# Performance work log

Hardware: AMD Instinct MI355X
Metric: run time of the kernel (lower is better)

The kernel has to match this reference:

```python
import jax, jax.numpy as jnp
import numpy as np

B, L, D, TK = 64, 48, 256, 128
T = 2 * L - 1  # L shifts + (L-1) reduces


def setup_inputs() -> dict:
    key = jax.random.key(0)
    ks = jax.random.split(key, 9)
    s = 0.05
    inp = {
        "buf_h": jax.random.normal(ks[0], (B, L, D), jnp.float32),
        "buf_c": jax.random.normal(ks[1], (B, L, D), jnp.float32),
        # Tracker weights: buf/stack1/stack2 (size -> 4*tracker_size, no bias), lateral (tk -> 4*tk, bias)
        "Wb": jax.random.normal(ks[2], (D, 4 * TK), jnp.float32) * s,
        "W1": jax.random.normal(ks[3], (D, 4 * TK), jnp.float32) * s,
        "W2": jax.random.normal(ks[4], (D, 4 * TK), jnp.float32) * s,
        "Wl": jax.random.normal(ks[5], (TK, 4 * TK), jnp.float32) * s,
        "bl": jnp.zeros((4 * TK,), jnp.float32),
        # Reduce (TreeLSTM) weights: left (size->5*size, bias), right (no bias), track (tk->5*size, no bias)
        "WL": jax.random.normal(ks[6], (D, 5 * D), jnp.float32) * s,
        "bL": jnp.zeros((5 * D,), jnp.float32),
        "WR": jax.random.normal(ks[7], (D, 5 * D), jnp.float32) * s,
        "WT": jax.random.normal(ks[8], (TK, 5 * D), jnp.float32) * s,
    }
    # Valid full-length transition sequence per example: S S (R S)*(L-2) R  -> SHIFT=0, REDUCE=1
    pat = np.array([0, 0] + [1, 0] * (L - 2) + [1], dtype=np.int32)
    inp["transitions"] = jnp.asarray(np.tile(pat[None], (B, 1)))  # [B, T]
    return inp


def _lstm(c, gates):
    # tracker LSTM cell: gates chunk into (a, i, f, o)
    a, i, f, o = jnp.split(gates, 4, axis=-1)
    c2 = jnp.tanh(a) * jax.nn.sigmoid(i) + jax.nn.sigmoid(f) * c
    h2 = jax.nn.sigmoid(o) * jnp.tanh(c2)
    return c2, h2


def _treelstm(c1, c2, gates):
    # Reduce composition: gates chunk into (a, i, f1, f2, o)
    a, i, f1, f2, o = jnp.split(gates, 5, axis=-1)
    c = jnp.tanh(a) * jax.nn.sigmoid(i) + jax.nn.sigmoid(f1) * c1 + jax.nn.sigmoid(f2) * c2
    h = jax.nn.sigmoid(o) * jnp.tanh(c)
    return h, c


def _spinn_forward(buf_h, buf_c, transitions, Wb, W1, W2, Wl, bl, WL, bL, WR, WT):
    Bn, Ln, Dn = buf_h.shape
    Tn = transitions.shape[1]
    bidx = jnp.arange(Bn)
    stack0 = jnp.zeros((Bn, Ln, 2 * Dn), buf_h.dtype)  # each slot holds [h; c]
    sp0 = jnp.zeros((Bn,), jnp.int32)  # stack depth
    bp0 = jnp.zeros((Bn,), jnp.int32)  # buffer read pointer
    th0 = jnp.zeros((Bn, Wl.shape[0]), buf_h.dtype)
    tc0 = jnp.zeros_like(th0)

    def top(stack_, sp_, k):
        # k-th item from the top, zeros if depth < k (matches explicit zero-padding)
        idx = jnp.clip(sp_ - k, 0, Ln - 1)
        v = stack_[bidx, idx]
        return jnp.where((sp_ >= k)[:, None], v, jnp.zeros_like(v))

    def step(carry, xs):
        stack, sp, bp, th, tc = carry
        t, trans = xs
        shift = (trans == 0)
        bp_safe = jnp.clip(bp, 0, Ln - 1)
        buf_ok = (bp < Ln)[:, None]
        tb_h = jnp.where(buf_ok, buf_h[bidx, bp_safe], 0.0)  # top-of-buffer h
        s1 = top(stack, sp, 1)
        s2 = top(stack, sp, 2)
        s1h, s1c = s1[:, :Dn], s1[:, Dn:]
        s2h, s2c = s2[:, :Dn], s2[:, Dn:]
        # Tracker: sum of three bias-free linears (+ lateral with bias after step 0)
        gates = tb_h @ Wb + s1h @ W1 + s2h @ W2
        gates = gates + jnp.where(t > 0, th @ Wl + bl, 0.0)
        tc2, th2 = _lstm(tc, gates)
        # Reduce: right = top of stack, left = second item; tracking = new tracker h
        rgates = s2h @ WL + bL + s1h @ WR + th2 @ WT
        rh, rc = _treelstm(s2c, s1c, rgates)
        reduced = jnp.concatenate([rh, rc], axis=-1)
        # Shift: push [h;c] from buffer
        tb_c = jnp.where(buf_ok, buf_c[bidx, bp_safe], 0.0)
        shifted = jnp.concatenate([tb_h, tb_c], axis=-1)
        newval = jnp.where(shift[:, None], shifted, reduced)
        pos = jnp.where(shift, sp, jnp.maximum(sp - 2, 0))
        stack = stack.at[bidx, pos].set(newval)
        sp = jnp.where(shift, sp + 1, jnp.maximum(sp - 1, 0))
        bp = bp + shift.astype(bp.dtype)
        return (stack, sp, bp, th2, tc2), None

    (stack, sp, bp, th, tc), _ = jax.lax.scan(
        step, (stack0, sp0, bp0, th0, tc0),
        (jnp.arange(Tn), transitions.T))
    final = stack[bidx, jnp.clip(sp - 1, 0, Ln - 1)]  # [B, 2D] = [h; c] of root
    return final


def reference(buf_h, buf_c, transitions, Wb, W1, W2, Wl, bl, WL, bL, WR, WT):
    return _spinn_forward(buf_h, buf_c, transitions, Wb, W1, W2, Wl, bl, WL, bL, WR, WT)
```

## Files before the change

kernel.cpp:

```cpp
#include <hip/hip_runtime.h>
#include <cstdint>
#include <cstddef>

#define NB 64
#define LN 48
#define DN 256
#define TKN 128
#define TN 95
#define RMAX 48
#define GA 512
#define GR 1280
#define NWG 256
#define NT 512

__device__ __forceinline__ float sigf(float x) { return 1.0f / (1.0f + expf(-x)); }

__device__ __forceinline__ float bf2f(unsigned u16) {
    unsigned x = u16 << 16;
    return __builtin_bit_cast(float, x);
}
__device__ __forceinline__ unsigned short f2bf(float f) {
    unsigned x = __builtin_bit_cast(unsigned, f);
    unsigned r = (x + 0x7FFFu + ((x >> 16) & 1u)) >> 16;
    return (unsigned short)r;
}

__device__ __forceinline__ float cohLd(const float* p) {
    return __hip_atomic_load(p, __ATOMIC_RELAXED, __HIP_MEMORY_SCOPE_AGENT);
}
__device__ __forceinline__ void cohSt(float* p, float v) {
    __hip_atomic_store(p, v, __ATOMIC_RELAXED, __HIP_MEMORY_SCOPE_AGENT);
}
__device__ __forceinline__ unsigned cohLdU(const unsigned* p) {
    return __hip_atomic_load(p, __ATOMIC_RELAXED, __HIP_MEMORY_SCOPE_AGENT);
}
__device__ __forceinline__ void cohStU(unsigned* p, unsigned v) {
    __hip_atomic_store(p, v, __ATOMIC_RELAXED, __HIP_MEMORY_SCOPE_AGENT);
}

__device__ __forceinline__ void qsync(unsigned* slots, int grp, unsigned& qph) {
    __syncthreads();
    qph += 1;
    if (threadIdx.x == 0) cohStU(&slots[blockIdx.x * 16], qph);
    if (threadIdx.x < 16) {
        while (cohLdU(&slots[(grp * 16 + threadIdx.x) * 16]) < qph)
            __builtin_amdgcn_s_sleep(1);
    }
    asm volatile("" ::: "memory");
    __syncthreads();
}

__device__ __forceinline__ void psync(unsigned* slotsP, int u, int xcd, unsigned& pph) {
    __syncthreads();
    pph += 1;
    if (threadIdx.x == 0) cohStU(&slotsP[(u * 8 + xcd) * 16], pph);
    if (threadIdx.x < 8) {
        while (cohLdU(&slotsP[(u * 8 + threadIdx.x) * 16]) < pph)
            __builtin_amdgcn_s_sleep(1);
    }
    asm volatile("" ::: "memory");
    __syncthreads();
}

__global__ void k_sched(const int* __restrict__ trans,
                        int* __restrict__ tbcode, int* __restrict__ s1code,
                        int* __restrict__ s2code, int* __restrict__ wkA,
                        int* __restrict__ fcode, int* __restrict__ anyred) {
    __shared__ int tg[NB][LN];
    int b = threadIdx.x;
    if (b >= NB) return;
    for (int i = 0; i < LN; ++i) tg[b][i] = -1;
    int sp = 0, bp = 0, k = 0;
    for (int t = 0; t < TN; ++t) {
        int tr = trans[b * TN + t];
        int shift = (tr == 0);
        int tb = (bp < LN) ? bp : -1;
        tbcode[t * NB + b] = tb;
        int i1 = sp - 1; if (i1 < 0) i1 = 0; if (i1 > LN - 1) i1 = LN - 1;
        int i2 = sp - 2; if (i2 < 0) i2 = 0; if (i2 > LN - 1) i2 = LN - 1;
        s1code[t * NB + b] = (sp >= 1) ? tg[b][i1] : -1;
        s2code[t * NB + b] = (sp >= 2) ? tg[b][i2] : -1;
        int wk_t;
        if (shift) {
            wk_t = -1;
            if (sp >= 0 && sp < LN) tg[b][sp] = tb;
            sp = sp + 1;
            bp = bp + 1;
        } else {
            wk_t = k;
            int pos = sp - 2; if (pos < 0) pos = 0;
            if (pos < LN) tg[b][pos] = 1000 + k;
            k++;
            sp = sp - 1; if (sp < 0) sp = 0;
        }
        wkA[t * NB + b] = wk_t;
        unsigned long long m = __ballot(wk_t >= 0);
        if (b == 0) anyred[t] = (m != 0ull) ? 1 : 0;
    }
    int fi = sp - 1; if (fi < 0) fi = 0; if (fi > LN - 1) fi = LN - 1;
    fcode[b] = tg[b][fi];
}

__global__ __launch_bounds__(256) void k_pack_a(
    const float* __restrict__ Wb, const float* __restrict__ W1,
    const float* __restrict__ W2, const float* __restrict__ Wl,
    const float* __restrict__ blv,
    unsigned short* __restrict__ WAb, float* __restrict__ blA) {
    int idx = blockIdx.x * 256 + threadIdx.x;
    if (idx < 8 * 896 * 64) {
        int s = idx / (896 * 64);
        int r = idx % (896 * 64);
        int k = r >> 6, c = r & 63;
        int p = s * 64 + c;
        int j = p >> 2, q = p & 3;
        int sc = q * 128 + j;
        float v;
        if (k < 256)      v = Wb[(size_t)k * GA + sc];
        else if (k < 512) v = W1[(size_t)(k - 256) * GA + sc];
        else if (k < 768) v = W2[(size_t)(k - 512) * GA + sc];
        else              v = Wl[(size_t)(k - 768) * GA + sc];
        WAb[idx] = f2bf(v);
    }
    if (idx < 512) {
        int j = idx >> 2, q = idx & 3;
        blA[idx] = blv[q * 128 + j];
    }
}

__global__ __launch_bounds__(256) void k_pack_b(
    const float* __restrict__ WLm, const float* __restrict__ WRm,
    const float* __restrict__ WTm, unsigned short* __restrict__ WBb) {
    int idx = blockIdx.x * 256 + threadIdx.x;
    if (idx >= 16 * 640 * 128) return;
    int s = idx / (640 * 128);
    int r = idx % (640 * 128);
    int k = r >> 7, cc = r & 127;
    int jj = cc >> 3, g = cc & 7;
    float v = 0.f;
    if (g < 5) {
        int sc = g * 256 + s * 16 + jj;
        if (k < 256)      v = WLm[(size_t)k * GR + sc];
        else if (k < 512) v = WRm[(size_t)(k - 256) * GR + sc];
        else              v = WTm[(size_t)(k - 512) * GR + sc];
    }
    WBb[idx] = f2bf(v);
}

__global__ __launch_bounds__(NT, 1) void k_spinn(
    const float* __restrict__ bufh, const float* __restrict__ bufc,
    const unsigned short* __restrict__ WAb, const float* __restrict__ blA,
    const unsigned short* __restrict__ WBb, const float* __restrict__ bLv,
    const int* __restrict__ tbcode, const int* __restrict__ s1code,
    const int* __restrict__ s2code, const int* __restrict__ wkA,
    const int* __restrict__ fcode, const int* __restrict__ anyred,
    float* __restrict__ th, float* __restrict__ tc,
    float* __restrict__ redh, float* __restrict__ redc,
    unsigned* __restrict__ slots, unsigned* __restrict__ slotsP,
    float* __restrict__ out) {
    const int wg = blockIdx.x;
    const int tid = threadIdx.x;
    const int lane = tid & 63;
    const int w = tid >> 6;
    unsigned qph = 0, pph = 0;

    const int xcd = wg & 7;
    const int u = wg >> 3;
    const int grp = wg >> 4;
    const int jg = xcd;
    const int bg1 = u;
    const int bg2 = u >> 1;
    const int jgw = (u & 1) + 2 * xcd;

    __shared__ float xs[2][896];
    __shared__ float part1[2][64][65];
    __shared__ float gsum[2][64];
    __shared__ float xs2[4][16][33];
    __shared__ float part2[16][16][21];
    __shared__ float gsum2[4][5][16];
    __shared__ float xst[4][128];
    __shared__ float cellv[2][4][17];

    for (int t = 0; t < TN; ++t) {
        const int par = t & 1;
        const bool red = anyred[t] != 0;

        int ngroups = red ? 1088 : 448;
        for (int g = tid; g < ngroups; g += NT) {
            if (g < 448) {
                int row = g & 1, k0 = (g >> 1) * 4;
                int b = bg1 * 2 + row;
                float4 v = {0.f, 0.f, 0.f, 0.f};
                if (k0 < 256) {
                    int c = tbcode[t * NB + b];
                    if (c >= 0) v = *(const float4*)&bufh[((size_t)b * LN + c) * DN + k0];
                } else if (k0 < 512) {
                    int c = s1code[t * NB + b];
                    int kk = k0 - 256;
                    if (c >= 1000) {
                        const float* p = &redh[((size_t)(c - 1000) * NB + b) * DN + kk];
                        v.x = cohLd(p); v.y = cohLd(p + 1); v.z = cohLd(p + 2); v.w = cohLd(p + 3);
                    } else if (c >= 0) v = *(const float4*)&bufh[((size_t)b * LN + c) * DN + kk];
                } else if (k0 < 768) {
                    int c = s2code[t * NB + b];
                    int kk = k0 - 512;
                    if (c >= 1000) {
                        const float* p = &redh[((size_t)(c - 1000) * NB + b) * DN + kk];
                        v.x = cohLd(p); v.y = cohLd(p + 1); v.z = cohLd(p + 2); v.w = cohLd(p + 3);
                    } else if (c >= 0) v = *(const float4*)&bufh[((size_t)b * LN + c) * DN + kk];
                } else {
                    const float* p = &th[((size_t)par * NB + b) * TKN + (k0 - 768)];
                    v.x = cohLd(p); v.y = cohLd(p + 1); v.z = cohLd(p + 2); v.w = cohLd(p + 3);
                }
                *(float4*)&xs[row][k0] = v;
            } else if (g < 960) {
                int g2 = g - 448;
                int row = g2 & 3, k0 = (g2 >> 2) * 4;
                int b = bg2 * 4 + row;
                float4 v = {0.f, 0.f, 0.f, 0.f};
                if (k0 < 256) {
                    int c = s2code[t * NB + b];
                    if (c >= 1000) {
                        const float* p = &redh[((size_t)(c - 1000) * NB + b) * DN + k0];
                        v.x = cohLd(p); v.y = cohLd(p + 1); v.z = cohLd(p + 2); v.w = cohLd(p + 3);
                    } else if (c >= 0) v = *(const float4*)&bufh[((size_t)b * LN + c) * DN + k0];
                } else {
                    int c = s1code[t * NB + b];
                    int kk = k0 - 256;
                    if (c >= 1000) {
                        const float* p = &redh[((size_t)(c - 1000) * NB + b) * DN + kk];
                        v.x = cohLd(p); v.y = cohLd(p + 1); v.z = cohLd(p + 2); v.w = cohLd(p + 3);
                    } else if (c >= 0) v = *(const float4*)&bufh[((size_t)b * LN + c) * DN + kk];
                }
                *(float4*)&xs2[row][k0 >> 5][k0 & 31] = v;
            } else {
                int g3 = g - 960;
                int sel = g3 >> 6, r = g3 & 63;
                int bl_ = r >> 4, jj = r & 15;
                int b = bg2 * 4 + bl_;
                int j = jgw * 16 + jj;
                int c = (sel ? s1code : s2code)[t * NB + b];
                float v = 0.f;
                if (c >= 1000)   v = redc[((size_t)(c - 1000) * NB + b) * DN + j];
                else if (c >= 0) v = bufc[((size_t)b * LN + c) * DN + j];
                cellv[sel][bl_][jj] = v;
            }
        }
        __syncthreads();

        float acc[5][4];
        if (w < 4 || !red) {
            int weff = w & 3, ihalf = w >> 2;
            int c8 = lane & 7, kq = lane >> 3;
            int kbase = weff * 224;
            int i0 = red ? 0 : ihalf * 14;
            int ni = red ? 28 : 14;
            const uint4* wp = (const uint4*)WAb + ((size_t)(jg * 896 + kbase + kq) * 8) + c8;
            float a0[8], a1[8];
            #pragma unroll
            for (int cc = 0; cc < 8; ++cc) { a0[cc] = 0.f; a1[cc] = 0.f; }
            #pragma unroll 4
            for (int ii = 0; ii < ni; ++ii) {
                int i = i0 + ii;
                uint4 wv = wp[(size_t)i * 64];
                int k = kbase + kq + i * 8;
                float x0 = xs[0][k], x1 = xs[1][k];
                float wf0 = bf2f(wv.x & 0xFFFF), wf1 = bf2f(wv.x >> 16);
                float wf2 = bf2f(wv.y & 0xFFFF), wf3 = bf2f(wv.y >> 16);
                float wf4 = bf2f(wv.z & 0xFFFF), wf5 = bf2f(wv.z >> 16);
                float wf6 = bf2f(wv.w & 0xFFFF), wf7 = bf2f(wv.w >> 16);
                a0[0] += x0 * wf0; a1[0] += x1 * wf0;
                a0[1] += x0 * wf1; a1[1] += x1 * wf1;
                a0[2] += x0 * wf2; a1[2] += x1 * wf2;
                a0[3] += x0 * wf3; a1[3] += x1 * wf3;
                a0[4] += x0 * wf4; a1[4] += x1 * wf4;
                a0[5] += x0 * wf5; a1[5] += x1 * wf5;
                a0[6] += x0 * wf6; a1[6] += x1 * wf6;
                a0[7] += x0 * wf7; a1[7] += x1 * wf7;
            }
            int slot = weff * 8 + kq + (red ? 0 : ihalf * 32);
            #pragma unroll
            for (int cc = 0; cc < 8; ++cc) {
                part1[0][c8 * 8 + cc][slot] = a0[cc];
                part1[1][c8 * 8 + cc][slot] = a1[cc];
            }
        } else {
            int t2 = tid - 256, jj = t2 & 15, ks = t2 >> 4;
            #pragma unroll
            for (int g = 0; g < 5; ++g)
                #pragma unroll
                for (int b4 = 0; b4 < 4; ++b4) acc[g][b4] = 0.f;
            const uint4* wb = (const uint4*)WBb + ((size_t)(jgw * 640 + ks * 32) * 16) + jj;
            #pragma unroll 4
            for (int i = 0; i < 32; ++i) {
                uint4 wv = wb[(size_t)i * 16];
                float w0 = bf2f(wv.x & 0xFFFF), w1 = bf2f(wv.x >> 16);
                float w2 = bf2f(wv.y & 0xFFFF), w3 = bf2f(wv.y >> 16);
                float w4 = bf2f(wv.z & 0xFFFF);
                float x0 = xs2[0][ks][i], x1 = xs2[1][ks][i];
                float x2 = xs2[2][ks][i], x3 = xs2[3][ks][i];
                acc[0][0] += x0 * w0; acc[1][0] += x0 * w1; acc[2][0] += x0 * w2; acc[3][0] += x0 * w3; acc[4][0] += x0 * w4;
                acc[0][1] += x1 * w0; acc[1][1] += x1 * w1; acc[2][1] += x1 * w2; acc[3][1] += x1 * w3; acc[4][1] += x1 * w4;
                acc[0][2] += x2 * w0; acc[1][2] += x2 * w1; acc[2][2] += x2 * w2; acc[3][2] += x2 * w3; acc[4][2] += x2 * w4;
                acc[0][3] += x3 * w0; acc[1][3] += x3 * w1; acc[2][3] += x3 * w2; acc[3][3] += x3 * w3; acc[4][3] += x3 * w4;
            }
        }
        __syncthreads();

        if (tid < 128) {
            int b = tid & 1, col = tid >> 1;
            float s = 0.f;
            #pragma unroll
            for (int ks = 0; ks < 32; ++ks) s += part1[b][col][ks];
            if (!red) {
                #pragma unroll
                for (int ks = 32; ks < 64; ++ks) s += part1[b][col][ks];
            }
            if (t > 0) s += blA[jg * 64 + col];
            gsum[b][col] = s;
        }
        __syncthreads();
        if (tid < 32) {
            int bl_ = tid >> 4, jj = tid & 15;
            int b = bg1 * 2 + bl_;
            int j = jg * 16 + jj;
            float4 g4 = *(const float4*)&gsum[bl_][jj * 4];
            float tco = tc[((size_t)par * NB + b) * TKN + j];
            float c2v = tanhf(g4.x) * sigf(g4.y) + sigf(g4.z) * tco;
            float h2 = sigf(g4.w) * tanhf(c2v);
            tc[((size_t)(par ^ 1) * NB + b) * TKN + j] = c2v;
            cohSt(&th[((size_t)(par ^ 1) * NB + b) * TKN + j], h2);
        }

        if (!red) {
            psync(slotsP, u, xcd, pph);
            continue;
        }
        qsync(slots, grp, qph);

        float xreg;
        {
            int b4 = tid >> 7, kk = tid & 127;
            xreg = cohLd(&th[((size_t)(par ^ 1) * NB + bg2 * 4 + b4) * TKN + kk]);
        }
        if (w >= 4) {
            int t2 = tid - 256, jj = t2 & 15, ks = t2 >> 4;
            #pragma unroll
            for (int g = 0; g < 5; ++g)
                #pragma unroll
                for (int b4 = 0; b4 < 4; ++b4)
                    part2[ks][jj][g * 4 + b4] = acc[g][b4];
        }
        {
            int b4 = tid >> 7, kk = tid & 127;
            xst[b4][kk] = xreg;
        }
        __syncthreads();
        if (w >= 4) {
            int t2 = tid - 256, jj = t2 & 15, ks = t2 >> 4;
            float wt[5][4];
            #pragma unroll
            for (int g = 0; g < 5; ++g)
                #pragma unroll
                for (int b4 = 0; b4 < 4; ++b4) wt[g][b4] = 0.f;
            const uint4* wb = (const uint4*)WBb + ((size_t)(jgw * 640 + 512 + ks * 8) * 16) + jj;
            #pragma unroll
            for (int i = 0; i < 8; ++i) {
                uint4 wv = wb[(size_t)i * 16];
                float w0 = bf2f(wv.x & 0xFFFF), w1 = bf2f(wv.x >> 16);
                float w2 = bf2f(wv.y & 0xFFFF), w3 = bf2f(wv.y >> 16);
                float w4 = bf2f(wv.z & 0xFFFF);
                int kk2 = ks * 8 + i;
                float x0 = xst[0][kk2], x1 = xst[1][kk2], x2 = xst[2][kk2], x3 = xst[3][kk2];
                wt[0][0] += x0 * w0; wt[1][0] += x0 * w1; wt[2][0] += x0 * w2; wt[3][0] += x0 * w3; wt[4][0] += x0 * w4;
                wt[0][1] += x1 * w0; wt[1][1] += x1 * w1; wt[2][1] += x1 * w2; wt[3][1] += x1 * w3; wt[4][1] += x1 * w4;
                wt[0][2] += x2 * w0; wt[1][2] += x2 * w1; wt[2][2] += x2 * w2; wt[3][2] += x2 * w3; wt[4][2] += x2 * w4;
                wt[0][3] += x3 * w0; wt[1][3] += x3 * w1; wt[2][3] += x3 * w2; wt[3][3] += x3 * w3; wt[4][3] += x3 * w4;
            }
            #pragma unroll
            for (int g = 0; g < 5; ++g)
                #pragma unroll
                for (int b4 = 0; b4 < 4; ++b4)
                    part2[ks][jj][g * 4 + b4] += wt[g][b4];
        }
        __syncthreads();
        if (tid < 320) {
            int g = tid >> 6, r = tid & 63;
            int bl_ = r >> 4, jj = r & 15;
            float s = 0.f;
            #pragma unroll
            for (int ks = 0; ks < 16; ++ks) s += part2[ks][jj][g * 4 + bl_];
            gsum2[bl_][g][jj] = s;
        }
        __syncthreads();
        if (tid < 64) {
            int bl_ = tid >> 4, jj = tid & 15;
            int b = bg2 * 4 + bl_;
            int wk = wkA[t * NB + b];
            if (wk >= 0) {
                int j = jgw * 16 + jj;
                float ga  = gsum2[bl_][0][jj] + bLv[0 * 256 + j];
                float gi  = gsum2[bl_][1][jj] + bLv[1 * 256 + j];
                float gf1 = gsum2[bl_][2][jj] + bLv[2 * 256 + j];
                float gf2 = gsum2[bl_][3][jj] + bLv[3 * 256 + j];
                float go  = gsum2[bl_][4][jj] + bLv[4 * 256 + j];
                float s2cv = cellv[0][bl_][jj];
                float s1cv = cellv[1][bl_][jj];
                float cc = tanhf(ga) * sigf(gi) + sigf(gf1) * s2cv + sigf(gf2) * s1cv;
                float hh = sigf(go) * tanhf(cc);
                cohSt(&redh[((size_t)wk * NB + b) * DN + j], hh);
                redc[((size_t)wk * NB + b) * DN + j] = cc;
            }
        }
        qsync(slots, grp, qph);
    }

    if (tid < 64) {
        int bl_ = tid >> 4, jj = tid & 15;
        int b = bg2 * 4 + bl_;
        int j = jgw * 16 + jj;
        int c = fcode[b];
        float h = 0.f, cv = 0.f;
        if (c >= 1000) {
            h  = cohLd(&redh[((size_t)(c - 1000) * NB + b) * DN + j]);
            cv = redc[((size_t)(c - 1000) * NB + b) * DN + j];
        } else if (c >= 0) {
            h  = bufh[((size_t)b * LN + c) * DN + j];
            cv = bufc[((size_t)b * LN + c) * DN + j];
        }
        out[(size_t)b * 2 * DN + j]      = h;
        out[(size_t)b * 2 * DN + DN + j] = cv;
    }
}

extern "C" void kernel_launch(void* const* d_in, const int* in_sizes, int n_in,
                              void* d_out, int out_size, void* d_ws, size_t ws_size,
                              hipStream_t stream) {
    const float* bufh = (const float*)d_in[0];
    const float* bufc = (const float*)d_in[1];
    const float* Wb   = (const float*)d_in[2];
    const float* W1   = (const float*)d_in[3];
    const float* W2   = (const float*)d_in[4];
    const float* Wl   = (const float*)d_in[5];
    const float* blv  = (const float*)d_in[6];
    const float* WLm  = (const float*)d_in[7];
    const float* bLv  = (const float*)d_in[8];
    const float* WR   = (const float*)d_in[9];
    const float* WT   = (const float*)d_in[10];
    const int* trans  = (const int*)d_in[11];
    float* out = (float*)d_out;

    char* p = (char*)d_ws;
    auto carve = [&](size_t bytes) -> char* {
        char* r = p;
        p += (bytes + 255) & ~(size_t)255;
        return r;
    };
    int* tbcode = (int*)carve((size_t)TN * NB * 4);
    int* s1code = (int*)carve((size_t)TN * NB * 4);
    int* s2code = (int*)carve((size_t)TN * NB * 4);
    int* wkA    = (int*)carve((size_t)TN * NB * 4);
    int* fcode  = (int*)carve((size_t)NB * 4);
    int* anyred = (int*)carve((size_t)TN * 4);
    float* th   = (float*)carve((size_t)2 * NB * TKN * 4);
    float* tc   = (float*)carve((size_t)2 * NB * TKN * 4);
    float* redh = (float*)carve((size_t)RMAX * NB * DN * 4);
    float* redc = (float*)carve((size_t)RMAX * NB * DN * 4);
    unsigned short* WAb = (unsigned short*)carve((size_t)8 * 896 * 64 * 2);
    float* blA  = (float*)carve((size_t)512 * 4);
    unsigned short* WBb = (unsigned short*)carve((size_t)16 * 640 * 128 * 2);
    unsigned* slots  = (unsigned*)carve((size_t)NWG * 16 * 4);
    unsigned* slotsP = (unsigned*)carve((size_t)NWG * 16 * 4);

    hipMemsetAsync(th, 0, (size_t)2 * NB * TKN * 4, stream);
    hipMemsetAsync(tc, 0, (size_t)2 * NB * TKN * 4, stream);
    hipMemsetAsync(slots, 0, (size_t)NWG * 16 * 4, stream);
    hipMemsetAsync(slotsP, 0, (size_t)NWG * 16 * 4, stream);

    k_sched<<<1, 64, 0, stream>>>(trans, tbcode, s1code, s2code, wkA, fcode, anyred);
    k_pack_a<<<(8 * 896 * 64 + 255) / 256, 256, 0, stream>>>(Wb, W1, W2, Wl, blv, WAb, blA);
    k_pack_b<<<(16 * 640 * 128 + 255) / 256, 256, 0, stream>>>(WLm, WR, WT, WBb);
    k_spinn<<<NWG, NT, 0, stream>>>(bufh, bufc, WAb, blA, WBb, bLv,
                                    tbcode, s1code, s2code, wkA, fcode, anyred,
                                    th, tc, redh, redc, slots, slotsP, out);
}
```

Measured before the change: 721.0 us.

## Prefetch step inputs before cross-workgroup barrier using precomputed readiness flags

The scheduler kernel now records, per step and example, whether each stack operand was produced at least two steps earlier (pre1/pre2). The main kernel moves the end-of-step barrier to the start of the next step and issues loads for already-ready buffer and reduce-result operands before spinning on the barrier, so their latency overlaps the wait. Only operands produced in the immediately preceding step and the tracker state are loaded after the barrier. This adds register pressure and extra schedule arrays, and it depends on the precomputed readiness being correct under the weaker sync ordering.

```diff
diff --git a/kernel.cpp b/kernel.cpp
--- a/kernel.cpp
+++ b/kernel.cpp
@@ -50,23 +50,13 @@
     __syncthreads();
 }
 
-__device__ __forceinline__ void psync(unsigned* slotsP, int u, int xcd, unsigned& pph) {
-    __syncthreads();
-    pph += 1;
-    if (threadIdx.x == 0) cohStU(&slotsP[(u * 8 + xcd) * 16], pph);
-    if (threadIdx.x < 8) {
-        while (cohLdU(&slotsP[(u * 8 + threadIdx.x) * 16]) < pph)
-            __builtin_amdgcn_s_sleep(1);
-    }
-    asm volatile("" ::: "memory");
-    __syncthreads();
-}
-
 __global__ void k_sched(const int* __restrict__ trans,
                         int* __restrict__ tbcode, int* __restrict__ s1code,
                         int* __restrict__ s2code, int* __restrict__ wkA,
-                        int* __restrict__ fcode, int* __restrict__ anyred) {
+                        int* __restrict__ fcode, int* __restrict__ anyred,
+                        int* __restrict__ pre1, int* __restrict__ pre2) {
     __shared__ int tg[NB][LN];
+    __shared__ short prod[NB][RMAX];
     int b = threadIdx.x;
     if (b >= NB) return;
     for (int i = 0; i < LN; ++i) tg[b][i] = -1;
@@ -78,8 +68,12 @@
         tbcode[t * NB + b] = tb;
         int i1 = sp - 1; if (i1 < 0) i1 = 0; if (i1 > LN - 1) i1 = LN - 1;
         int i2 = sp - 2; if (i2 < 0) i2 = 0; if (i2 > LN - 1) i2 = LN - 1;
-        s1code[t * NB + b] = (sp >= 1) ? tg[b][i1] : -1;
-        s2code[t * NB + b] = (sp >= 2) ? tg[b][i2] : -1;
+        int c1 = (sp >= 1) ? tg[b][i1] : -1;
+        int c2 = (sp >= 2) ? tg[b][i2] : -1;
+        s1code[t * NB + b] = c1;
+        s2code[t * NB + b] = c2;
+        pre1[t * NB + b] = (c1 < 1000) ? 1 : ((int)prod[b][c1 - 1000] <= t - 2 ? 1 : 0);
+        pre2[t * NB + b] = (c2 < 1000) ? 1 : ((int)prod[b][c2 - 1000] <= t - 2 ? 1 : 0);
         int wk_t;
         if (shift) {
             wk_t = -1;
@@ -88,6 +82,7 @@
             bp = bp + 1;
         } else {
             wk_t = k;
+            prod[b][k] = (short)t;
             int pos = sp - 2; if (pos < 0) pos = 0;
             if (pos < LN) tg[b][pos] = 1000 + k;
             k++;
@@ -146,6 +141,75 @@
     WBb[idx] = f2bf(v);
 }
 
+__device__ __forceinline__ int pf_try(
+    int g, int t, int bg1, int bg2,
+    const int* __restrict__ tbcode, const int* __restrict__ s1code,
+    const int* __restrict__ s2code,
+    const int* __restrict__ pre1, const int* __restrict__ pre2,
+    const float* __restrict__ bufh, const float* __restrict__ redh,
+    float4& v) {
+    v = float4{0.f, 0.f, 0.f, 0.f};
+    if (g < 448) {
+        int row = g & 1, k0 = (g >> 1) * 4;
+        int b = bg1 * 2 + row;
+        if (k0 < 256) {
+            int c = tbcode[t * NB + b];
+            if (c >= 0) v = *(const float4*)&bufh[((size_t)b * LN + c) * DN + k0];
+            return 1;
+        } else if (k0 < 512) {
+            int c = s1code[t * NB + b];
+            int kk = k0 - 256;
+            if (c >= 1000) {
+                if (!pre1[t * NB + b]) return 0;
+                const float* p = &redh[((size_t)(c - 1000) * NB + b) * DN + kk];
+                v.x = cohLd(p); v.y = cohLd(p + 1); v.z = cohLd(p + 2); v.w = cohLd(p + 3);
+                return 1;
+            }
+            if (c >= 0) v = *(const float4*)&bufh[((size_t)b * LN + c) * DN + kk];
+            return 1;
+        } else if (k0 < 768) {
+            int c = s2code[t * NB + b];
+            int kk = k0 - 512;
+            if (c >= 1000) {
+                if (!pre2[t * NB + b]) return 0;
+                const float* p = &redh[((size_t)(c - 1000) * NB + b) * DN + kk];
+                v.x = cohLd(p); v.y = cohLd(p + 1); v.z = cohLd(p + 2); v.w = cohLd(p + 3);
+                return 1;
+            }
+            if (c >= 0) v = *(const float4*)&bufh[((size_t)b * LN + c) * DN + kk];
+            return 1;
+        }
+        return 0;
+    } else if (g < 960) {
+        int g2 = g - 448;
+        int row = g2 & 3, k0 = (g2 >> 2) * 4;
+        int b = bg2 * 4 + row;
+        if (k0 < 256) {
+            int c = s2code[t * NB + b];
+            if (c >= 1000) {
+                if (!pre2[t * NB + b]) return 0;
+                const float* p = &redh[((size_t)(c - 1000) * NB + b) * DN + k0];
+                v.x = cohLd(p); v.y = cohLd(p + 1); v.z = cohLd(p + 2); v.w = cohLd(p + 3);
+                return 1;
+            }
+            if (c >= 0) v = *(const float4*)&bufh[((size_t)b * LN + c) * DN + k0];
+            return 1;
+        } else {
+            int c = s1code[t * NB + b];
+            int kk = k0 - 256;
+            if (c >= 1000) {
+                if (!pre1[t * NB + b]) return 0;
+                const float* p = &redh[((size_t)(c - 1000) * NB + b) * DN + kk];
+                v.x = cohLd(p); v.y = cohLd(p + 1); v.z = cohLd(p + 2); v.w = cohLd(p + 3);
+                return 1;
+            }
+            if (c >= 0) v = *(const float4*)&bufh[((size_t)b * LN + c) * DN + kk];
+            return 1;
+        }
+    }
+    return 0;
+}
+
 __global__ __launch_bounds__(NT, 1) void k_spinn(
     const float* __restrict__ bufh, const float* __restrict__ bufc,
     const unsigned short* __restrict__ WAb, const float* __restrict__ blA,
@@ -153,6 +217,7 @@
     const int* __restrict__ tbcode, const int* __restrict__ s1code,
     const int* __restrict__ s2code, const int* __restrict__ wkA,
     const int* __restrict__ fcode, const int* __restrict__ anyred,
+    const int* __restrict__ pre1, const int* __restrict__ pre2,
     float* __restrict__ th, float* __restrict__ tc,
     float* __restrict__ redh, float* __restrict__ redc,
     unsigned* __restrict__ slots, unsigned* __restrict__ slotsP,
@@ -180,56 +245,103 @@
     __shared__ float xst[4][128];
     __shared__ float cellv[2][4][17];
 
+    bool prevRed = false;
     for (int t = 0; t < TN; ++t) {
         const int par = t & 1;
         const bool red = anyred[t] != 0;
-
-        int ngroups = red ? 1088 : 448;
-        for (int g = tid; g < ngroups; g += NT) {
+        const int ngroups = red ? 1088 : 448;
+
+        float4 pf0, pf1, pf2;
+        int hv0 = 0, hv1 = 0, hv2 = 0;
+
+        if (t > 0) {
+            __syncthreads();
+            {
+                int g = tid;
+                if (g < ngroups) hv0 = pf_try(g, t, bg1, bg2, tbcode, s1code, s2code,
+                                              pre1, pre2, bufh, redh, pf0);
+                g = tid + NT;
+                if (g < ngroups) hv1 = pf_try(g, t, bg1, bg2, tbcode, s1code, s2code,
+                                              pre1, pre2, bufh, redh, pf1);
+                g = tid + 2 * NT;
+                if (g < ngroups) hv2 = pf_try(g, t, bg1, bg2, tbcode, s1code, s2code,
+                                              pre1, pre2, bufh, redh, pf2);
+            }
+            if (prevRed) {
+                qph += 1;
+                if (tid == 0) cohStU(&slots[wg * 16], qph);
+                if (tid < 16) {
+                    while (cohLdU(&slots[(grp * 16 + tid) * 16]) < qph)
+                        __builtin_amdgcn_s_sleep(1);
+                }
+            } else {
+                pph += 1;
+                if (tid == 0) cohStU(&slotsP[(u * 8 + xcd) * 16], pph);
+                if (tid < 8) {
+                    while (cohLdU(&slotsP[(u * 8 + tid) * 16]) < pph)
+                        __builtin_amdgcn_s_sleep(1);
+                }
+            }
+            asm volatile("" ::: "memory");
+            __syncthreads();
+        }
+        prevRed = red;
+
+        #pragma unroll
+        for (int idx = 0; idx < 3; ++idx) {
+            int g = tid + idx * NT;
+            if (g >= ngroups) continue;
+            int hv = (idx == 0) ? hv0 : (idx == 1) ? hv1 : hv2;
+            float4 pv = (idx == 0) ? pf0 : (idx == 1) ? pf1 : pf2;
             if (g < 448) {
                 int row = g & 1, k0 = (g >> 1) * 4;
-                int b = bg1 * 2 + row;
-                float4 v = {0.f, 0.f, 0.f, 0.f};
-                if (k0 < 256) {
-                    int c = tbcode[t * NB + b];
-                    if (c >= 0) v = *(const float4*)&bufh[((size_t)b * LN + c) * DN + k0];
-                } else if (k0 < 512) {
-                    int c = s1code[t * NB + b];
-                    int kk = k0 - 256;
-                    if (c >= 1000) {
-                        const float* p = &redh[((size_t)(c - 1000) * NB + b) * DN + kk];
+                float4 v;
+                if (hv) v = pv;
+                else {
+                    int b = bg1 * 2 + row;
+                    v = float4{0.f, 0.f, 0.f, 0.f};
+                    if (k0 < 512 && k0 >= 256) {
+                        int c = s1code[t * NB + b];
+                        int kk = k0 - 256;
+                        if (c >= 1000) {
+                            const float* p = &redh[((size_t)(c - 1000) * NB + b) * DN + kk];
+                            v.x = cohLd(p); v.y = cohLd(p + 1); v.z = cohLd(p + 2); v.w = cohLd(p + 3);
+                        }
+                    } else if (k0 < 768 && k0 >= 512) {
+                        int c = s2code[t * NB + b];
+                        int kk = k0 - 512;
+                        if (c >= 1000) {
+                            const float* p = &redh[((size_t)(c - 1000) * NB + b) * DN + kk];
+                            v.x = cohLd(p); v.y = cohLd(p + 1); v.z = cohLd(p + 2); v.w = cohLd(p + 3);
+                        }
+                    } else if (k0 >= 768) {
+                        const float* p = &th[((size_t)par * NB + b) * TKN + (k0 - 768)];
                         v.x = cohLd(p); v.y = cohLd(p + 1); v.z = cohLd(p + 2); v.w = cohLd(p + 3);
-                    } else if (c >= 0) v = *(const float4*)&bufh[((size_t)b * LN + c) * DN + kk];
-                } else if (k0 < 768) {
-                    int c = s2code[t * NB + b];
-                    int kk = k0 - 512;
-                    if (c >= 1000) {
-                        const float* p = &redh[((size_t)(c - 1000) * NB + b) * DN + kk];
-                        v.x = cohLd(p); v.y = cohLd(p + 1); v.z = cohLd(p + 2); v.w = cohLd(p + 3);
-                    } else if (c >= 0) v = *(const float4*)&bufh[((size_t)b * LN + c) * DN + kk];
-                } else {
-                    const float* p = &th[((size_t)par * NB + b) * TKN + (k0 - 768)];
-                    v.x = cohLd(p); v.y = cohLd(p + 1); v.z = cohLd(p + 2); v.w = cohLd(p + 3);
+                    }
                 }
                 *(float4*)&xs[row][k0] = v;
             } else if (g < 960) {
                 int g2 = g - 448;
                 int row = g2 & 3, k0 = (g2 >> 2) * 4;
-                int b = bg2 * 4 + row;
-                float4 v = {0.f, 0.f, 0.f, 0.f};
-                if (k0 < 256) {
-                    int c = s2code[t * NB + b];
-                    if (c >= 1000) {
-                        const float* p = &redh[((size_t)(c - 1000) * NB + b) * DN + k0];
-                        v.x = cohLd(p); v.y = cohLd(p + 1); v.z = cohLd(p + 2); v.w = cohLd(p + 3);
-                    } else if (c >= 0) v = *(const float4*)&bufh[((size_t)b * LN + c) * DN + k0];
-                } else {
-                    int c = s1code[t * NB + b];
-                    int kk = k0 - 256;
-                    if (c >= 1000) {
-                        const float* p = &redh[((size_t)(c - 1000) * NB + b) * DN + kk];
-                        v.x = cohLd(p); v.y = cohLd(p + 1); v.z = cohLd(p + 2); v.w = cohLd(p + 3);
-                    } else if (c >= 0) v = *(const float4*)&bufh[((size_t)b * LN + c) * DN + kk];
+                float4 v;
+                if (hv) v = pv;
+                else {
+                    int b = bg2 * 4 + row;
+                    v = float4{0.f, 0.f, 0.f, 0.f};
+                    if (k0 < 256) {
+                        int c = s2code[t * NB + b];
+                        if (c >= 1000) {
+                            const float* p = &redh[((size_t)(c - 1000) * NB + b) * DN + k0];
+                            v.x = cohLd(p); v.y = cohLd(p + 1); v.z = cohLd(p + 2); v.w = cohLd(p + 3);
+                        }
+                    } else {
+                        int c = s1code[t * NB + b];
+                        int kk = k0 - 256;
+                        if (c >= 1000) {
+                            const float* p = &redh[((size_t)(c - 1000) * NB + b) * DN + kk];
+                            v.x = cohLd(p); v.y = cohLd(p + 1); v.z = cohLd(p + 2); v.w = cohLd(p + 3);
+                        }
+                    }
                 }
                 *(float4*)&xs2[row][k0 >> 5][k0 & 31] = v;
             } else {
@@ -331,10 +443,8 @@
             cohSt(&th[((size_t)(par ^ 1) * NB + b) * TKN + j], h2);
         }
 
-        if (!red) {
-            psync(slotsP, u, xcd, pph);
-            continue;
-        }
+        if (!red) continue;
+
         qsync(slots, grp, qph);
 
         float xreg;
@@ -411,8 +521,9 @@
                 redc[((size_t)wk * NB + b) * DN + j] = cc;
             }
         }
-        qsync(slots, grp, qph);
-    }
+    }
+
+    qsync(slots, grp, qph);
 
     if (tid < 64) {
         int bl_ = tid >> 4, jj = tid & 15;
@@ -461,6 +572,8 @@
     int* wkA    = (int*)carve((size_t)TN * NB * 4);
     int* fcode  = (int*)carve((size_t)NB * 4);
     int* anyred = (int*)carve((size_t)TN * 4);
+    int* pre1   = (int*)carve((size_t)TN * NB * 4);
+    int* pre2   = (int*)carve((size_t)TN * NB * 4);
     float* th   = (float*)carve((size_t)2 * NB * TKN * 4);
     float* tc   = (float*)carve((size_t)2 * NB * TKN * 4);
     float* redh = (float*)carve((size_t)RMAX * NB * DN * 4);
@@ -476,10 +589,11 @@
     hipMemsetAsync(slots, 0, (size_t)NWG * 16 * 4, stream);
     hipMemsetAsync(slotsP, 0, (size_t)NWG * 16 * 4, stream);
 
-    k_sched<<<1, 64, 0, stream>>>(trans, tbcode, s1code, s2code, wkA, fcode, anyred);
+    k_sched<<<1, 64, 0, stream>>>(trans, tbcode, s1code, s2code, wkA, fcode, anyred, pre1, pre2);
     k_pack_a<<<(8 * 896 * 64 + 255) / 256, 256, 0, stream>>>(Wb, W1, W2, Wl, blv, WAb, blA);
     k_pack_b<<<(16 * 640 * 128 + 255) / 256, 256, 0, stream>>>(WLm, WR, WT, WBb);
     k_spinn<<<NWG, NT, 0, stream>>>(bufh, bufc, WAb, blA, WBb, bLv,
                                     tbcode, s1code, s2code, wkA, fcode, anyred,
+                                    pre1, pre2,
                                     th, tc, redh, redc, slots, slotsP, out);
 }
```

New measurement: 867.0 us. 1.2x slower.
